# Optimization experiments

Hardware: AMD Instinct MI355X
Metric: run time of the kernel (lower is better)

## Reference

```python
import jax, jax.numpy as jnp
import numpy as np

U, P, D, H, E = 512, 1024, 128, 256, 98304
N = U + P


def setup_inputs() -> dict:
    key = jax.random.key(0)
    ks = jax.random.split(key, 16)
    def nrm(k, shape, scale=0.05):
        return jax.random.normal(k, shape, jnp.float32) * scale
    z = lambda *s: jnp.zeros(s, jnp.float32)
    return {
        "user_ids": jnp.arange(U),
        "paper_ids": jnp.arange(P),
        "edge_index": jax.random.randint(ks[0], (2, E), 0, N),
        "user_paper_interactions": jax.random.uniform(ks[1], (U, P), jnp.float32),
        "user_emb": nrm(ks[2], (U, D), 1.0),   # nn.Embedding tables
        "paper_emb": nrm(ks[3], (P, D), 1.0),
        "W0": nrm(ks[4], (D, H)), "b0": z(H),   # GCNConv weights (stored [in,out])
        "W1": nrm(ks[5], (H, H)), "b1": z(H),
        "W2": nrm(ks[6], (H, H)), "b2": z(H),
        "Wu": nrm(ks[7], (H, D)), "bu": z(D),   # user_output Linear
        "Wp": nrm(ks[8], (H, D)), "bp": z(D),   # paper_output Linear
        "Wq1": nrm(ks[9], (2 * D, H)), "bq1": z(H),  # predictor Linear 1
        "Wq2": nrm(ks[10], (H, 1)), "bq2": z(1),      # predictor Linear 2
    }


def gcn_conv(x, src, dst, W, b):
    """PyG GCNConv: add self-loops, symmetric D^-1/2 (A+I) D^-1/2 normalization."""
    n = x.shape[0]
    loop = jnp.arange(n)
    s = jnp.concatenate([src, loop])
    d = jnp.concatenate([dst, loop])
    deg = jax.ops.segment_sum(jnp.ones(d.shape, x.dtype), d, num_segments=n)
    dis = jnp.where(deg > 0, jax.lax.rsqrt(jnp.maximum(deg, 1.0)), 0.0)
    norm = dis[s] * dis[d]                      # [E+n]
    h = x @ W                                   # [n, H]
    out = jax.ops.segment_sum(h[s] * norm[:, None], d, num_segments=n)
    return out + b


def reference(user_ids, paper_ids, edge_index, user_paper_interactions,
              user_emb, paper_emb, W0, b0, W1, b1, W2, b2,
              Wu, bu, Wp, bp, Wq1, bq1, Wq2, bq2):
    # embedding lookups + node feature matrix [U+P, D]
    x = jnp.concatenate([user_emb[user_ids], paper_emb[paper_ids]], axis=0)
    src, dst = edge_index[0], edge_index[1]
    for W, b in ((W0, b0), (W1, b1), (W2, b2)):
        x = jax.nn.relu(gcn_conv(x, src, dst, W, b))  # dropout is identity in eval
    nu = user_ids.shape[0]
    np_ = paper_ids.shape[0]
    user_final = x[:nu] @ Wu + bu               # [U, D]
    paper_final = x[nu:] @ Wp + bp              # [P, D]
    # broadcast outer-product concat -> [U, P, 2D]
    combined = jnp.concatenate([
        jnp.broadcast_to(user_final[:, None, :], (nu, np_, user_final.shape[-1])),
        jnp.broadcast_to(paper_final[None, :, :], (nu, np_, paper_final.shape[-1])),
    ], axis=-1)
    h = jax.nn.relu(combined @ Wq1 + bq1)       # [U, P, H]
    pred = jax.nn.sigmoid(h @ Wq2 + bq2)[..., 0]  # [U, P]
    return pred
```

## Files before the change

### kernel.cpp

```cpp
#include <hip/hip_runtime.h>
#include <math.h>

constexpr int Uc = 512;
constexpr int Pc = 1024;
constexpr int Dc = 128;
constexpr int Hc = 256;
constexpr int Ec = 98304;
constexpr int Nc = 1536;
constexpr int CAP = 192;

__device__ __forceinline__ void fma4(float4& a, float n, const float4 r) {
    a.x += n * r.x; a.y += n * r.y; a.z += n * r.z; a.w += n * r.w;
}

template <int K>
__device__ __forceinline__ void gemm_core16(const float* __restrict__ xr,
                                            const float* __restrict__ wc, int M,
                                            float& acc0, float& acc1) {
#pragma unroll 4
    for (int k = 0; k < K; k += 4) {
        float4 a = *(const float4*)(xr + k);
        float2 b0 = *(const float2*)(wc + (size_t)k * M);
        float2 b1 = *(const float2*)(wc + (size_t)(k + 1) * M);
        float2 b2 = *(const float2*)(wc + (size_t)(k + 2) * M);
        float2 b3 = *(const float2*)(wc + (size_t)(k + 3) * M);
        acc0 += a.x * b0.x; acc1 += a.x * b0.y;
        acc0 += a.y * b1.x; acc1 += a.y * b1.y;
        acc0 += a.z * b2.x; acc1 += a.z * b2.y;
        acc0 += a.w * b3.x; acc1 += a.w * b3.y;
    }
}

__global__ void k_front(const int* __restrict__ e_src, const int* __restrict__ e_dst,
                        int* __restrict__ cnt, int* __restrict__ colF,
                        const float* __restrict__ Wu, const float* __restrict__ Wp,
                        const float* __restrict__ Wq1, const float* __restrict__ bu,
                        const float* __restrict__ bp, const float* __restrict__ bq1,
                        float* __restrict__ Wup, float* __restrict__ Wpp,
                        float* __restrict__ bvu, float* __restrict__ bvp) {
    int t = threadIdx.x, b = blockIdx.x;
    if (b < 384) {
        int e = b * 256 + t;
        int d = e_dst[e];
        int pos = atomicAdd(&cnt[d], 1);
        if (pos < CAP) colF[d * CAP + pos] = e_src[e];
    } else if (b < 640) {
        int id = b - 384;
        int z = id >> 7, tile = id & 127;
        int tx = t & 15, ty = t >> 4;
        const float* X = z ? Wp : Wu;
        const float* W = Wq1 + (z ? (size_t)Dc * Hc : 0);
        float* Y = z ? Wpp : Wup;
        int row = (tile >> 3) * 16 + ty, col = (tile & 7) * 32 + tx * 2;
        float a0 = 0.f, a1 = 0.f;
        gemm_core16<Dc>(X + (size_t)row * Dc, W + col, Hc, a0, a1);
        *(float2*)&Y[(size_t)row * Hc + col] = make_float2(a0, a1);
    } else if (b == 640) {
        float s = bq1[t];
#pragma unroll 8
        for (int d = 0; d < Dc; d++) s += bu[d] * Wq1[d * Hc + t];
        bvu[t] = s;
    } else {
        float s = 0.f;
#pragma unroll 8
        for (int d = 0; d < Dc; d++) s += bp[d] * Wq1[(Dc + d) * Hc + t];
        bvp[t] = s;
    }
}

__global__ void __launch_bounds__(256) k_l0(
        const int* __restrict__ uid, const int* __restrict__ pid,
        const float* __restrict__ ue, const float* __restrict__ pe,
        const float* __restrict__ W0, const float* __restrict__ b0,
        const int* __restrict__ cnt, const int* __restrict__ colF,
        float* __restrict__ out) {
    __shared__ const float* sptr[2][CAP];
    __shared__ float snrm[2][CAP];
    __shared__ __align__(16) float pagg[4][Dc];
    __shared__ __align__(16) float aggT[Dc][2];
    __shared__ __align__(16) float red[4][2][Hc];
    int t = threadIdx.x, b = blockIdx.x;
    int ibase = b * 2;
    int c[2]; float di[2];
#pragma unroll
    for (int r = 0; r < 2; r++) {
        c[r] = cnt[ibase + r];
        di[r] = rsqrtf((float)(c[r] + 1));
        int deg = min(c[r], CAP);
        if (t < deg) {
            int s = colF[(ibase + r) * CAP + t];
            sptr[r][t] = (s < Uc) ? ue + (size_t)uid[s] * Dc
                                  : pe + (size_t)pid[s - Uc] * Dc;
            snrm[r][t] = rsqrtf((float)(cnt[s] + 1));
        }
    }
    __syncthreads();
    {
        int wv = t >> 6, ln = t & 63;
        int r = wv >> 1, h = wv & 1;
        int i = ibase + r;
        int dg = min(c[r], CAP);
        int dg2 = dg >> 1;
        int j0 = h ? dg2 : 0, j1 = h ? dg : dg2;
        float2 acc = make_float2(0.f, 0.f);
        if (h == 0) {
            const float* xi = (i < Uc) ? ue + (size_t)uid[i] * Dc
                                       : pe + (size_t)pid[i - Uc] * Dc;
            float2 a2 = *(const float2*)(xi + ln * 2);
            acc.x = di[r] * a2.x;
            acc.y = di[r] * a2.y;
        }
        int j = j0;
        for (; j + 8 <= j1; j += 8) {
            float n0 = snrm[r][j],     n1 = snrm[r][j + 1];
            float n2 = snrm[r][j + 2], n3 = snrm[r][j + 3];
            float n4 = snrm[r][j + 4], n5 = snrm[r][j + 5];
            float n6 = snrm[r][j + 6], n7 = snrm[r][j + 7];
            float2 r0 = *(const float2*)(sptr[r][j]     + ln * 2);
            float2 r1 = *(const float2*)(sptr[r][j + 1] + ln * 2);
            float2 r2 = *(const float2*)(sptr[r][j + 2] + ln * 2);
            float2 r3 = *(const float2*)(sptr[r][j + 3] + ln * 2);
            float2 r4 = *(const float2*)(sptr[r][j + 4] + ln * 2);
            float2 r5 = *(const float2*)(sptr[r][j + 5] + ln * 2);
            float2 r6 = *(const float2*)(sptr[r][j + 6] + ln * 2);
            float2 r7 = *(const float2*)(sptr[r][j + 7] + ln * 2);
            acc.x += n0 * r0.x + n1 * r1.x + n2 * r2.x + n3 * r3.x;
            acc.y += n0 * r0.y + n1 * r1.y + n2 * r2.y + n3 * r3.y;
            acc.x += n4 * r4.x + n5 * r5.x + n6 * r6.x + n7 * r7.x;
            acc.y += n4 * r4.y + n5 * r5.y + n6 * r6.y + n7 * r7.y;
        }
        for (; j + 4 <= j1; j += 4) {
            float n0 = snrm[r][j],     n1 = snrm[r][j + 1];
            float n2 = snrm[r][j + 2], n3 = snrm[r][j + 3];
            float2 r0 = *(const float2*)(sptr[r][j]     + ln * 2);
            float2 r1 = *(const float2*)(sptr[r][j + 1] + ln * 2);
            float2 r2 = *(const float2*)(sptr[r][j + 2] + ln * 2);
            float2 r3 = *(const float2*)(sptr[r][j + 3] + ln * 2);
            acc.x += n0 * r0.x + n1 * r1.x + n2 * r2.x + n3 * r3.x;
            acc.y += n0 * r0.y + n1 * r1.y + n2 * r2.y + n3 * r3.y;
        }
        for (; j < j1; j++) {
            float2 r0 = *(const float2*)(sptr[r][j] + ln * 2);
            acc.x += snrm[r][j] * r0.x;
            acc.y += snrm[r][j] * r0.y;
        }
        pagg[wv][ln * 2]     = acc.x;
        pagg[wv][ln * 2 + 1] = acc.y;
    }
    __syncthreads();
    {
        int r = t >> 7, f = t & 127;
        aggT[f][r] = di[r] * (pagg[2 * r][f] + pagg[2 * r + 1][f]);
    }
    __syncthreads();
    {
        int wv = t >> 6, ln = t & 63;
        int k0 = wv * (Dc / 4);
        float4 a0 = {0.f, 0.f, 0.f, 0.f}, a1 = {0.f, 0.f, 0.f, 0.f};
        const float* Wp_ = W0 + (size_t)k0 * Hc + ln * 4;
#pragma unroll 8
        for (int kk = 0; kk < Dc / 4; kk++) {
            float2 g = *(const float2*)&aggT[k0 + kk][0];
            float4 w = *(const float4*)(Wp_ + (size_t)kk * Hc);
            a0.x += g.x * w.x; a0.y += g.x * w.y; a0.z += g.x * w.z; a0.w += g.x * w.w;
            a1.x += g.y * w.x; a1.y += g.y * w.y; a1.z += g.y * w.z; a1.w += g.y * w.w;
        }
        *(float4*)&red[wv][0][ln * 4] = a0;
        *(float4*)&red[wv][1][ln * 4] = a1;
    }
    __syncthreads();
    {
        float bb = b0[t];
        float s0 = (red[0][0][t] + red[1][0][t]) + (red[2][0][t] + red[3][0][t]) + bb;
        float s1 = (red[0][1][t] + red[1][1][t]) + (red[2][1][t] + red[3][1][t]) + bb;
        out[(size_t)(ibase + 0) * Hc + t] = fmaxf(s0, 0.f);
        out[(size_t)(ibase + 1) * Hc + t] = fmaxf(s1, 0.f);
    }
}

__device__ __forceinline__ void agg_wave2(const float* __restrict__ X,
                                          const int (*sidx)[CAP], const float (*snrm)[CAP],
                                          const int* c, const float* di, int ibase,
                                          float (*pagg)[Hc], int t) {
    int wv = t >> 6, ln = t & 63;
    int r = wv >> 1, h = wv & 1;
    int dg = min(c[r], CAP);
    int dg2 = dg >> 1;
    int j0 = h ? dg2 : 0, j1 = h ? dg : dg2;
    float4 acc = make_float4(0.f, 0.f, 0.f, 0.f);
    if (h == 0) {
        acc = *(const float4*)&X[(size_t)(ibase + r) * Hc + ln * 4];
        acc.x *= di[r]; acc.y *= di[r]; acc.z *= di[r]; acc.w *= di[r];
    }
    int j = j0;
    for (; j + 8 <= j1; j += 8) {
        float n0 = snrm[r][j],     n1 = snrm[r][j + 1];
        float n2 = snrm[r][j + 2], n3 = snrm[r][j + 3];
        float n4 = snrm[r][j + 4], n5 = snrm[r][j + 5];
        float n6 = snrm[r][j + 6], n7 = snrm[r][j + 7];
        float4 r0 = *(const float4*)&X[sidx[r][j]     + ln * 4];
        float4 r1 = *(const float4*)&X[sidx[r][j + 1] + ln * 4];
        float4 r2 = *(const float4*)&X[sidx[r][j + 2] + ln * 4];
        float4 r3 = *(const float4*)&X[sidx[r][j + 3] + ln * 4];
        float4 r4 = *(const float4*)&X[sidx[r][j + 4] + ln * 4];
        float4 r5 = *(const float4*)&X[sidx[r][j + 5] + ln * 4];
        float4 r6 = *(const float4*)&X[sidx[r][j + 6] + ln * 4];
        float4 r7 = *(const float4*)&X[sidx[r][j + 7] + ln * 4];
        fma4(acc, n0, r0); fma4(acc, n1, r1); fma4(acc, n2, r2); fma4(acc, n3, r3);
        fma4(acc, n4, r4); fma4(acc, n5, r5); fma4(acc, n6, r6); fma4(acc, n7, r7);
    }
    for (; j + 4 <= j1; j += 4) {
        float n0 = snrm[r][j],     n1 = snrm[r][j + 1];
        float n2 = snrm[r][j + 2], n3 = snrm[r][j + 3];
        float4 r0 = *(const float4*)&X[sidx[r][j]     + ln * 4];
        float4 r1 = *(const float4*)&X[sidx[r][j + 1] + ln * 4];
        float4 r2 = *(const float4*)&X[sidx[r][j + 2] + ln * 4];
        float4 r3 = *(const float4*)&X[sidx[r][j + 3] + ln * 4];
        fma4(acc, n0, r0); fma4(acc, n1, r1); fma4(acc, n2, r2); fma4(acc, n3, r3);
    }
    for (; j < j1; j++) {
        float4 r0 = *(const float4*)&X[sidx[r][j] + ln * 4];
        fma4(acc, snrm[r][j], r0);
    }
    *(float4*)&pagg[wv][ln * 4] = acc;
}

__device__ __forceinline__ void gemv_wsplit(const float (*aggT)[2],
                                            const float* __restrict__ W,
                                            float (*red)[2][Hc], int t) {
    int wv = t >> 6, ln = t & 63;
    int k0 = wv * (Hc / 4);
    float4 a0 = {0.f, 0.f, 0.f, 0.f}, a1 = {0.f, 0.f, 0.f, 0.f};
    const float* Wp_ = W + (size_t)k0 * Hc + ln * 4;
#pragma unroll 8
    for (int kk = 0; kk < Hc / 4; kk++) {
        float2 g = *(const float2*)&aggT[k0 + kk][0];
        float4 w = *(const float4*)(Wp_ + (size_t)kk * Hc);
        a0.x += g.x * w.x; a0.y += g.x * w.y; a0.z += g.x * w.z; a0.w += g.x * w.w;
        a1.x += g.y * w.x; a1.y += g.y * w.y; a1.z += g.y * w.z; a1.w += g.y * w.w;
    }
    *(float4*)&red[wv][0][ln * 4] = a0;
    *(float4*)&red[wv][1][ln * 4] = a1;
}

__global__ void __launch_bounds__(256) k_lh(
        const float* __restrict__ X, const float* __restrict__ W,
        const float* __restrict__ bias, const int* __restrict__ cnt,
        const int* __restrict__ colF, float* __restrict__ out) {
    __shared__ int sidx[2][CAP];
    __shared__ float snrm[2][CAP];
    __shared__ __align__(16) float pagg[4][Hc];
    __shared__ __align__(16) float aggT[Hc][2];
    __shared__ __align__(16) float red[4][2][Hc];
    int t = threadIdx.x, b = blockIdx.x;
    int ibase = b * 2;
    int c[2]; float di[2];
#pragma unroll
    for (int r = 0; r < 2; r++) {
        c[r] = cnt[ibase + r];
        di[r] = rsqrtf((float)(c[r] + 1));
        int deg = min(c[r], CAP);
        if (t < deg) {
            int s = colF[(ibase + r) * CAP + t];
            sidx[r][t] = s * Hc;
            snrm[r][t] = rsqrtf((float)(cnt[s] + 1));
        }
    }
    __syncthreads();
    agg_wave2(X, sidx, snrm, c, di, ibase, pagg, t);
    __syncthreads();
    *(float2*)&aggT[t][0] = make_float2(di[0] * (pagg[0][t] + pagg[1][t]),
                                        di[1] * (pagg[2][t] + pagg[3][t]));
    __syncthreads();
    gemv_wsplit(aggT, W, red, t);
    __syncthreads();
    {
        float bb = bias[t];
        float s0 = (red[0][0][t] + red[1][0][t]) + (red[2][0][t] + red[3][0][t]) + bb;
        float s1 = (red[0][1][t] + red[1][1][t]) + (red[2][1][t] + red[3][1][t]) + bb;
        out[(size_t)(ibase + 0) * Hc + t] = fmaxf(s0, 0.f);
        out[(size_t)(ibase + 1) * Hc + t] = fmaxf(s1, 0.f);
    }
}

__global__ void __launch_bounds__(256) k_lht(
        const float* __restrict__ X, const float* __restrict__ W2,
        const float* __restrict__ b2, const int* __restrict__ cnt,
        const int* __restrict__ colF,
        const float* __restrict__ Wup, const float* __restrict__ Wpp,
        const float* __restrict__ bvu, const float* __restrict__ bvp,
        float* __restrict__ AuT, float* __restrict__ ApT) {
    __shared__ int sidx[2][CAP];
    __shared__ float snrm[2][CAP];
    __shared__ __align__(16) float pagg[4][Hc];
    __shared__ __align__(16) float aggT[Hc][2];
    __shared__ __align__(16) float xlocT[Hc][2];
    __shared__ __align__(16) float red[4][2][Hc];
    int t = threadIdx.x, b = blockIdx.x;
    int ibase = b * 2;
    int c[2]; float di[2];
#pragma unroll
    for (int r = 0; r < 2; r++) {
        c[r] = cnt[ibase + r];
        di[r] = rsqrtf((float)(c[r] + 1));
        int deg = min(c[r], CAP);
        if (t < deg) {
            int s = colF[(ibase + r) * CAP + t];
            sidx[r][t] = s * Hc;
            snrm[r][t] = rsqrtf((float)(cnt[s] + 1));
        }
    }
    __syncthreads();
    agg_wave2(X, sidx, snrm, c, di, ibase, pagg, t);
    __syncthreads();
    *(float2*)&aggT[t][0] = make_float2(di[0] * (pagg[0][t] + pagg[1][t]),
                                        di[1] * (pagg[2][t] + pagg[3][t]));
    __syncthreads();
    gemv_wsplit(aggT, W2, red, t);
    __syncthreads();
    {
        float bb = b2[t];
        float s0 = (red[0][0][t] + red[1][0][t]) + (red[2][0][t] + red[3][0][t]) + bb;
        float s1 = (red[0][1][t] + red[1][1][t]) + (red[2][1][t] + red[3][1][t]) + bb;
        *(float2*)&xlocT[t][0] = make_float2(fmaxf(s0, 0.f), fmaxf(s1, 0.f));
    }
    __syncthreads();
    {
        const float* Wsel = (b < 256) ? Wup : Wpp;
        gemv_wsplit(xlocT, Wsel, red, t);
    }
    __syncthreads();
    {
        const float* bsel = (b < 256) ? bvu : bvp;
        float* YT  = (b < 256) ? AuT : ApT;
        int ldy    = (b < 256) ? Uc : Pc;
        int rloc   = (b < 256) ? ibase : ibase - Uc;
        float bb = bsel[t];
        float s0 = (red[0][0][t] + red[1][0][t]) + (red[2][0][t] + red[3][0][t]) + bb;
        float s1 = (red[0][1][t] + red[1][1][t]) + (red[2][1][t] + red[3][1][t]) + bb;
        *(float2*)&YT[(size_t)t * ldy + rloc] = make_float2(s0, s1);
    }
}

__global__ void __launch_bounds__(256) k_pred(
        const float* __restrict__ AuT, const float* __restrict__ ApT,
        const float* __restrict__ Wq2, const float* __restrict__ bq2,
        float* __restrict__ out) {
    __shared__ float auS[Hc * 8];
    int t = threadIdx.x;
    int ub = blockIdx.x * 8, pb = blockIdx.y * 256;
#pragma unroll
    for (int i = t; i < Hc * 8; i += 256) {
        int k = i >> 3, u = i & 7;
        auS[i] = AuT[(size_t)k * Uc + ub + u];
    }
    __syncthreads();
    int wv = t >> 6, ln = t & 63;
    const float* app = ApT + pb + ln * 4;
    const float* aup = auS + wv * 2;
    float acc[2][4] = {};
#pragma unroll 4
    for (int k = 0; k < Hc; k++) {
        float w = Wq2[k];
        float2 a = *(const float2*)(aup + k * 8);
        float4 p = *(const float4*)(app + (size_t)k * Pc);
        acc[0][0] += fmaxf(a.x + p.x, 0.f) * w;
        acc[0][1] += fmaxf(a.x + p.y, 0.f) * w;
        acc[0][2] += fmaxf(a.x + p.z, 0.f) * w;
        acc[0][3] += fmaxf(a.x + p.w, 0.f) * w;
        acc[1][0] += fmaxf(a.y + p.x, 0.f) * w;
        acc[1][1] += fmaxf(a.y + p.y, 0.f) * w;
        acc[1][2] += fmaxf(a.y + p.z, 0.f) * w;
        acc[1][3] += fmaxf(a.y + p.w, 0.f) * w;
    }
    float bq = bq2[0];
#pragma unroll
    for (int r = 0; r < 2; r++) {
        int u = ub + wv * 2 + r;
        float4 o;
        o.x = 1.f / (1.f + __expf(-(acc[r][0] + bq)));
        o.y = 1.f / (1.f + __expf(-(acc[r][1] + bq)));
        o.z = 1.f / (1.f + __expf(-(acc[r][2] + bq)));
        o.w = 1.f / (1.f + __expf(-(acc[r][3] + bq)));
        *(float4*)&out[(size_t)u * Pc + pb + ln * 4] = o;
    }
}


extern "C" void kernel_launch(void* const* d_in, const int* in_sizes, int n_in,
                              void* d_out, int out_size, void* d_ws, size_t ws_size,
                              hipStream_t stream) {
    const int*   uid = (const int*)d_in[0];
    const int*   pid = (const int*)d_in[1];
    const int*   ei  = (const int*)d_in[2];
    const float* ue  = (const float*)d_in[4];
    const float* pe  = (const float*)d_in[5];
    const float* W0  = (const float*)d_in[6];  const float* b0 = (const float*)d_in[7];
    const float* W1  = (const float*)d_in[8];  const float* b1 = (const float*)d_in[9];
    const float* W2  = (const float*)d_in[10]; const float* b2 = (const float*)d_in[11];
    const float* Wu  = (const float*)d_in[12]; const float* bu = (const float*)d_in[13];
    const float* Wp  = (const float*)d_in[14]; const float* bp = (const float*)d_in[15];
    const float* Wq1 = (const float*)d_in[16]; const float* bq1 = (const float*)d_in[17];
    const float* Wq2 = (const float*)d_in[18]; const float* bq2 = (const float*)d_in[19];

    const int* e_src = ei;
    const int* e_dst = ei + Ec;

    char* w = (char*)d_ws;
    auto alloc = [&](size_t bytes) { char* p = w; w += (bytes + 255) & ~size_t(255); return p; };
    int*   cnt  = (int*)alloc(Nc * 4);
    int*   colF = (int*)alloc((size_t)Nc * CAP * 4);
    float* xA   = (float*)alloc((size_t)Nc * Hc * 4);
    float* xB   = (float*)alloc((size_t)Nc * Hc * 4);
    float* Wup  = (float*)alloc((size_t)Hc * Hc * 4);
    float* Wpp  = (float*)alloc((size_t)Hc * Hc * 4);
    float* bvu  = (float*)alloc(Hc * 4);
    float* bvp  = (float*)alloc(Hc * 4);
    float* AuT  = (float*)alloc((size_t)Hc * Uc * 4);
    float* ApT  = (float*)alloc((size_t)Hc * Pc * 4);
    float* pred = (float*)d_out;

    hipMemsetAsync(cnt, 0, Nc * 4, stream);
    k_front<<<642, 256, 0, stream>>>(e_src, e_dst, cnt, colF, Wu, Wp, Wq1,
                                     bu, bp, bq1, Wup, Wpp, bvu, bvp);
    k_l0<<<Nc / 2, 256, 0, stream>>>(uid, pid, ue, pe, W0, b0, cnt, colF, xA);
    k_lh<<<Nc / 2, 256, 0, stream>>>(xA, W1, b1, cnt, colF, xB);
    k_lht<<<Nc / 2, 256, 0, stream>>>(xB, W2, b2, cnt, colF, Wup, Wpp, bvu, bvp, AuT, ApT);
    k_pred<<<dim3(Uc / 8, Pc / 256), 256, 0, stream>>>(AuT, ApT, Wq2, bq2, pred);
}
```

Before: 192.6 us.

## Fuse all GCN stages into one persistent cooperative kernel with grid syncs

```diff
diff --git a/kernel.cpp b/kernel.cpp
--- a/kernel.cpp
+++ b/kernel.cpp
@@ -1,5 +1,8 @@
 #include <hip/hip_runtime.h>
+#include <hip/hip_cooperative_groups.h>
 #include <math.h>
+
+namespace cg = cooperative_groups;
 
 constexpr int Uc = 512;
 constexpr int Pc = 1024;
@@ -12,6 +15,27 @@
 __device__ __forceinline__ void fma4(float4& a, float n, const float4 r) {
     a.x += n * r.x; a.y += n * r.y; a.z += n * r.z; a.w += n * r.w;
 }
+
+union __align__(16) SharedU {
+    struct {
+        const float* sptr[2][CAP];
+        float snrm[2][CAP];
+        float pagg[4][Dc];
+        float aggT[Dc][2];
+        float red[4][2][Hc];
+    } l0;
+    struct {
+        int sidx[2][CAP];
+        float snrm[2][CAP];
+        float pagg[4][Hc];
+        float aggT[Hc][2];
+        float xlocT[Hc][2];
+        float red[4][2][Hc];
+    } lh;
+    struct {
+        float auS[Hc * 8];
+    } pr;
+};
 
 template <int K>
 __device__ __forceinline__ void gemm_core16(const float* __restrict__ xr,
@@ -31,14 +55,15 @@
     }
 }
 
-__global__ void k_front(const int* __restrict__ e_src, const int* __restrict__ e_dst,
-                        int* __restrict__ cnt, int* __restrict__ colF,
-                        const float* __restrict__ Wu, const float* __restrict__ Wp,
-                        const float* __restrict__ Wq1, const float* __restrict__ bu,
-                        const float* __restrict__ bp, const float* __restrict__ bq1,
-                        float* __restrict__ Wup, float* __restrict__ Wpp,
-                        float* __restrict__ bvu, float* __restrict__ bvp) {
-    int t = threadIdx.x, b = blockIdx.x;
+__device__ __forceinline__ void phase_front(
+        int b, int t,
+        const int* __restrict__ e_src, const int* __restrict__ e_dst,
+        int* __restrict__ cnt, int* __restrict__ colF,
+        const float* __restrict__ Wu, const float* __restrict__ Wp,
+        const float* __restrict__ Wq1, const float* __restrict__ bu,
+        const float* __restrict__ bp, const float* __restrict__ bq1,
+        float* __restrict__ Wup, float* __restrict__ Wpp,
+        float* __restrict__ bvu, float* __restrict__ bvp) {
     if (b < 384) {
         int e = b * 256 + t;
         int d = e_dst[e];
@@ -60,7 +85,7 @@
 #pragma unroll 8
         for (int d = 0; d < Dc; d++) s += bu[d] * Wq1[d * Hc + t];
         bvu[t] = s;
-    } else {
+    } else if (b == 641) {
         float s = 0.f;
 #pragma unroll 8
         for (int d = 0; d < Dc; d++) s += bp[d] * Wq1[(Dc + d) * Hc + t];
@@ -68,18 +93,12 @@
     }
 }
 
-__global__ void __launch_bounds__(256) k_l0(
+__device__ void phase_l0(SharedU& su, int b, int t,
         const int* __restrict__ uid, const int* __restrict__ pid,
         const float* __restrict__ ue, const float* __restrict__ pe,
         const float* __restrict__ W0, const float* __restrict__ b0,
         const int* __restrict__ cnt, const int* __restrict__ colF,
         float* __restrict__ out) {
-    __shared__ const float* sptr[2][CAP];
-    __shared__ float snrm[2][CAP];
-    __shared__ __align__(16) float pagg[4][Dc];
-    __shared__ __align__(16) float aggT[Dc][2];
-    __shared__ __align__(16) float red[4][2][Hc];
-    int t = threadIdx.x, b = blockIdx.x;
     int ibase = b * 2;
     int c[2]; float di[2];
 #pragma unroll
@@ -89,9 +108,9 @@
         int deg = min(c[r], CAP);
         if (t < deg) {
             int s = colF[(ibase + r) * CAP + t];
-            sptr[r][t] = (s < Uc) ? ue + (size_t)uid[s] * Dc
-                                  : pe + (size_t)pid[s - Uc] * Dc;
-            snrm[r][t] = rsqrtf((float)(cnt[s] + 1));
+            su.l0.sptr[r][t] = (s < Uc) ? ue + (size_t)uid[s] * Dc
+                                        : pe + (size_t)pid[s - Uc] * Dc;
+            su.l0.snrm[r][t] = rsqrtf((float)(cnt[s] + 1));
         }
     }
     __syncthreads();
@@ -112,45 +131,45 @@
         }
         int j = j0;
         for (; j + 8 <= j1; j += 8) {
-            float n0 = snrm[r][j],     n1 = snrm[r][j + 1];
-            float n2 = snrm[r][j + 2], n3 = snrm[r][j + 3];
-            float n4 = snrm[r][j + 4], n5 = snrm[r][j + 5];
-            float n6 = snrm[r][j + 6], n7 = snrm[r][j + 7];
-            float2 r0 = *(const float2*)(sptr[r][j]     + ln * 2);
-            float2 r1 = *(const float2*)(sptr[r][j + 1] + ln * 2);
-            float2 r2 = *(const float2*)(sptr[r][j + 2] + ln * 2);
-            float2 r3 = *(const float2*)(sptr[r][j + 3] + ln * 2);
-            float2 r4 = *(const float2*)(sptr[r][j + 4] + ln * 2);
-            float2 r5 = *(const float2*)(sptr[r][j + 5] + ln * 2);
-            float2 r6 = *(const float2*)(sptr[r][j + 6] + ln * 2);
-            float2 r7 = *(const float2*)(sptr[r][j + 7] + ln * 2);
+            float n0 = su.l0.snrm[r][j],     n1 = su.l0.snrm[r][j + 1];
+            float n2 = su.l0.snrm[r][j + 2], n3 = su.l0.snrm[r][j + 3];
+            float n4 = su.l0.snrm[r][j + 4], n5 = su.l0.snrm[r][j + 5];
+            float n6 = su.l0.snrm[r][j + 6], n7 = su.l0.snrm[r][j + 7];
+            float2 r0 = *(const float2*)(su.l0.sptr[r][j]     + ln * 2);
+            float2 r1 = *(const float2*)(su.l0.sptr[r][j + 1] + ln * 2);
+            float2 r2 = *(const float2*)(su.l0.sptr[r][j + 2] + ln * 2);
+            float2 r3 = *(const float2*)(su.l0.sptr[r][j + 3] + ln * 2);
+            float2 r4 = *(const float2*)(su.l0.sptr[r][j + 4] + ln * 2);
+            float2 r5 = *(const float2*)(su.l0.sptr[r][j + 5] + ln * 2);
+            float2 r6 = *(const float2*)(su.l0.sptr[r][j + 6] + ln * 2);
+            float2 r7 = *(const float2*)(su.l0.sptr[r][j + 7] + ln * 2);
             acc.x += n0 * r0.x + n1 * r1.x + n2 * r2.x + n3 * r3.x;
             acc.y += n0 * r0.y + n1 * r1.y + n2 * r2.y + n3 * r3.y;
             acc.x += n4 * r4.x + n5 * r5.x + n6 * r6.x + n7 * r7.x;
             acc.y += n4 * r4.y + n5 * r5.y + n6 * r6.y + n7 * r7.y;
         }
         for (; j + 4 <= j1; j += 4) {
-            float n0 = snrm[r][j],     n1 = snrm[r][j + 1];
-            float n2 = snrm[r][j + 2], n3 = snrm[r][j + 3];
-            float2 r0 = *(const float2*)(sptr[r][j]     + ln * 2);
-            float2 r1 = *(const float2*)(sptr[r][j + 1] + ln * 2);
-            float2 r2 = *(const float2*)(sptr[r][j + 2] + ln * 2);
-            float2 r3 = *(const float2*)(sptr[r][j + 3] + ln * 2);
+            float n0 = su.l0.snrm[r][j],     n1 = su.l0.snrm[r][j + 1];
+            float n2 = su.l0.snrm[r][j + 2], n3 = su.l0.snrm[r][j + 3];
+            float2 r0 = *(const float2*)(su.l0.sptr[r][j]     + ln * 2);
+            float2 r1 = *(const float2*)(su.l0.sptr[r][j + 1] + ln * 2);
+            float2 r2 = *(const float2*)(su.l0.sptr[r][j + 2] + ln * 2);
+            float2 r3 = *(const float2*)(su.l0.sptr[r][j + 3] + ln * 2);
             acc.x += n0 * r0.x + n1 * r1.x + n2 * r2.x + n3 * r3.x;
             acc.y += n0 * r0.y + n1 * r1.y + n2 * r2.y + n3 * r3.y;
         }
         for (; j < j1; j++) {
-            float2 r0 = *(const float2*)(sptr[r][j] + ln * 2);
-            acc.x += snrm[r][j] * r0.x;
-            acc.y += snrm[r][j] * r0.y;
-        }
-        pagg[wv][ln * 2]     = acc.x;
-        pagg[wv][ln * 2 + 1] = acc.y;
+            float2 r0 = *(const float2*)(su.l0.sptr[r][j] + ln * 2);
+            acc.x += su.l0.snrm[r][j] * r0.x;
+            acc.y += su.l0.snrm[r][j] * r0.y;
+        }
+        su.l0.pagg[wv][ln * 2]     = acc.x;
+        su.l0.pagg[wv][ln * 2 + 1] = acc.y;
     }
     __syncthreads();
     {
         int r = t >> 7, f = t & 127;
-        aggT[f][r] = di[r] * (pagg[2 * r][f] + pagg[2 * r + 1][f]);
+        su.l0.aggT[f][r] = di[r] * (su.l0.pagg[2 * r][f] + su.l0.pagg[2 * r + 1][f]);
     }
     __syncthreads();
     {
@@ -160,19 +179,21 @@
         const float* Wp_ = W0 + (size_t)k0 * Hc + ln * 4;
 #pragma unroll 8
         for (int kk = 0; kk < Dc / 4; kk++) {
-            float2 g = *(const float2*)&aggT[k0 + kk][0];
+            float2 g = *(const float2*)&su.l0.aggT[k0 + kk][0];
             float4 w = *(const float4*)(Wp_ + (size_t)kk * Hc);
             a0.x += g.x * w.x; a0.y += g.x * w.y; a0.z += g.x * w.z; a0.w += g.x * w.w;
             a1.x += g.y * w.x; a1.y += g.y * w.y; a1.z += g.y * w.z; a1.w += g.y * w.w;
         }
-        *(float4*)&red[wv][0][ln * 4] = a0;
-        *(float4*)&red[wv][1][ln * 4] = a1;
+        *(float4*)&su.l0.red[wv][0][ln * 4] = a0;
+        *(float4*)&su.l0.red[wv][1][ln * 4] = a1;
     }
     __syncthreads();
     {
         float bb = b0[t];
-        float s0 = (red[0][0][t] + red[1][0][t]) + (red[2][0][t] + red[3][0][t]) + bb;
-        float s1 = (red[0][1][t] + red[1][1][t]) + (red[2][1][t] + red[3][1][t]) + bb;
+        float s0 = (su.l0.red[0][0][t] + su.l0.red[1][0][t]) +
+                   (su.l0.red[2][0][t] + su.l0.red[3][0][t]) + bb;
+        float s1 = (su.l0.red[0][1][t] + su.l0.red[1][1][t]) +
+                   (su.l0.red[2][1][t] + su.l0.red[3][1][t]) + bb;
         out[(size_t)(ibase + 0) * Hc + t] = fmaxf(s0, 0.f);
         out[(size_t)(ibase + 1) * Hc + t] = fmaxf(s1, 0.f);
     }
@@ -243,18 +264,10 @@
     *(float4*)&red[wv][1][ln * 4] = a1;
 }
 
-__global__ void __launch_bounds__(256) k_lh(
-        const float* __restrict__ X, const float* __restrict__ W,
-        const float* __restrict__ bias, const int* __restrict__ cnt,
-        const int* __restrict__ colF, float* __restrict__ out) {
-    __shared__ int sidx[2][CAP];
-    __shared__ float snrm[2][CAP];
-    __shared__ __align__(16) float pagg[4][Hc];
-    __shared__ __align__(16) float aggT[Hc][2];
-    __shared__ __align__(16) float red[4][2][Hc];
-    int t = threadIdx.x, b = blockIdx.x;
+__device__ __forceinline__ void layer_head(SharedU& su, int b, int t,
+        const float* __restrict__ X, const int* __restrict__ cnt,
+        const int* __restrict__ colF, int* c, float* di) {
     int ibase = b * 2;
-    int c[2]; float di[2];
 #pragma unroll
     for (int r = 0; r < 2; r++) {
         c[r] = cnt[ibase + r];
@@ -262,25 +275,168 @@
         int deg = min(c[r], CAP);
         if (t < deg) {
             int s = colF[(ibase + r) * CAP + t];
-            sidx[r][t] = s * Hc;
-            snrm[r][t] = rsqrtf((float)(cnt[s] + 1));
-        }
-    }
-    __syncthreads();
-    agg_wave2(X, sidx, snrm, c, di, ibase, pagg, t);
-    __syncthreads();
-    *(float2*)&aggT[t][0] = make_float2(di[0] * (pagg[0][t] + pagg[1][t]),
-                                        di[1] * (pagg[2][t] + pagg[3][t]));
-    __syncthreads();
-    gemv_wsplit(aggT, W, red, t);
-    __syncthreads();
-    {
-        float bb = bias[t];
-        float s0 = (red[0][0][t] + red[1][0][t]) + (red[2][0][t] + red[3][0][t]) + bb;
-        float s1 = (red[0][1][t] + red[1][1][t]) + (red[2][1][t] + red[3][1][t]) + bb;
-        out[(size_t)(ibase + 0) * Hc + t] = fmaxf(s0, 0.f);
-        out[(size_t)(ibase + 1) * Hc + t] = fmaxf(s1, 0.f);
-    }
+            su.lh.sidx[r][t] = s * Hc;
+            su.lh.snrm[r][t] = rsqrtf((float)(cnt[s] + 1));
+        }
+    }
+    __syncthreads();
+    agg_wave2(X, su.lh.sidx, su.lh.snrm, c, di, ibase, su.lh.pagg, t);
+    __syncthreads();
+    *(float2*)&su.lh.aggT[t][0] =
+        make_float2(di[0] * (su.lh.pagg[0][t] + su.lh.pagg[1][t]),
+                    di[1] * (su.lh.pagg[2][t] + su.lh.pagg[3][t]));
+    __syncthreads();
+}
+
+__device__ void phase_lh(SharedU& su, int b, int t,
+        const float* __restrict__ X, const float* __restrict__ W,
+        const float* __restrict__ bias, const int* __restrict__ cnt,
+        const int* __restrict__ colF, float* __restrict__ out) {
+    int c[2]; float di[2];
+    layer_head(su, b, t, X, cnt, colF, c, di);
+    gemv_wsplit(su.lh.aggT, W, su.lh.red, t);
+    __syncthreads();
+    int ibase = b * 2;
+    float bb = bias[t];
+    float s0 = (su.lh.red[0][0][t] + su.lh.red[1][0][t]) +
+               (su.lh.red[2][0][t] + su.lh.red[3][0][t]) + bb;
+    float s1 = (su.lh.red[0][1][t] + su.lh.red[1][1][t]) +
+               (su.lh.red[2][1][t] + su.lh.red[3][1][t]) + bb;
+    out[(size_t)(ibase + 0) * Hc + t] = fmaxf(s0, 0.f);
+    out[(size_t)(ibase + 1) * Hc + t] = fmaxf(s1, 0.f);
+}
+
+__device__ void phase_lht(SharedU& su, int b, int t,
+        const float* __restrict__ X, const float* __restrict__ W2,
+        const float* __restrict__ b2, const int* __restrict__ cnt,
+        const int* __restrict__ colF,
+        const float* __restrict__ Wup, const float* __restrict__ Wpp,
+        const float* __restrict__ bvu, const float* __restrict__ bvp,
+        float* __restrict__ AuT, float* __restrict__ ApT) {
+    int c[2]; float di[2];
+    layer_head(su, b, t, X, cnt, colF, c, di);
+    gemv_wsplit(su.lh.aggT, W2, su.lh.red, t);
+    __syncthreads();
+    {
+        float bb = b2[t];
+        float s0 = (su.lh.red[0][0][t] + su.lh.red[1][0][t]) +
+                   (su.lh.red[2][0][t] + su.lh.red[3][0][t]) + bb;
+        float s1 = (su.lh.red[0][1][t] + su.lh.red[1][1][t]) +
+                   (su.lh.red[2][1][t] + su.lh.red[3][1][t]) + bb;
+        *(float2*)&su.lh.xlocT[t][0] = make_float2(fmaxf(s0, 0.f), fmaxf(s1, 0.f));
+    }
+    __syncthreads();
+    gemv_wsplit(su.lh.xlocT, (b < 256) ? Wup : Wpp, su.lh.red, t);
+    __syncthreads();
+    {
+        int ibase = b * 2;
+        const float* bsel = (b < 256) ? bvu : bvp;
+        float* YT  = (b < 256) ? AuT : ApT;
+        int ldy    = (b < 256) ? Uc : Pc;
+        int rloc   = (b < 256) ? ibase : ibase - Uc;
+        float bb = bsel[t];
+        float s0 = (su.lh.red[0][0][t] + su.lh.red[1][0][t]) +
+                   (su.lh.red[2][0][t] + su.lh.red[3][0][t]) + bb;
+        float s1 = (su.lh.red[0][1][t] + su.lh.red[1][1][t]) +
+                   (su.lh.red[2][1][t] + su.lh.red[3][1][t]) + bb;
+        *(float2*)&YT[(size_t)t * ldy + rloc] = make_float2(s0, s1);
+    }
+}
+
+__device__ void phase_pred(float* auS, int b, int t,
+        const float* __restrict__ AuT, const float* __restrict__ ApT,
+        const float* __restrict__ Wq2, const float* __restrict__ bq2,
+        float* __restrict__ out) {
+    int ub = (b >> 3) * 8, pb = (b & 7) * 128;
+#pragma unroll
+    for (int i = t; i < Hc * 8; i += 256) {
+        int k = i >> 3, u = i & 7;
+        auS[i] = AuT[(size_t)k * Uc + ub + u];
+    }
+    __syncthreads();
+    int wv = t >> 6, ln = t & 63;
+    const float* app = ApT + pb + ln * 2;
+    const float* aup = auS + wv * 2;
+    float acc[2][2] = {};
+#pragma unroll 4
+    for (int k = 0; k < Hc; k++) {
+        float w = Wq2[k];
+        float2 a = *(const float2*)(aup + k * 8);
+        float2 p = *(const float2*)(app + (size_t)k * Pc);
+        acc[0][0] += fmaxf(a.x + p.x, 0.f) * w;
+        acc[0][1] += fmaxf(a.x + p.y, 0.f) * w;
+        acc[1][0] += fmaxf(a.y + p.x, 0.f) * w;
+        acc[1][1] += fmaxf(a.y + p.y, 0.f) * w;
+    }
+    float bq = bq2[0];
+#pragma unroll
+    for (int r = 0; r < 2; r++) {
+        int u = ub + wv * 2 + r;
+        float2 o;
+        o.x = 1.f / (1.f + __expf(-(acc[r][0] + bq)));
+        o.y = 1.f / (1.f + __expf(-(acc[r][1] + bq)));
+        *(float2*)&out[(size_t)u * Pc + pb + ln * 2] = o;
+    }
+}
+
+struct KArgs {
+    const int *uid, *pid, *e_src, *e_dst;
+    const float *ue, *pe;
+    const float *W0, *b0, *W1, *b1, *W2, *b2;
+    const float *Wu, *bu, *Wp, *bp, *Wq1, *bq1, *Wq2, *bq2;
+    int *cnt, *colF;
+    float *xA, *xB, *Wup, *Wpp, *bvu, *bvp, *AuT, *ApT, *pred;
+};
+
+__global__ void __launch_bounds__(256, 3) k_all(KArgs A) {
+    cg::grid_group g = cg::this_grid();
+    __shared__ SharedU su;
+    int t = threadIdx.x, b = blockIdx.x;
+    {
+        int i = b * 256 + t;
+        if (i < Nc) A.cnt[i] = 0;
+    }
+    g.sync();
+    phase_front(b, t, A.e_src, A.e_dst, A.cnt, A.colF, A.Wu, A.Wp, A.Wq1,
+                A.bu, A.bp, A.bq1, A.Wup, A.Wpp, A.bvu, A.bvp);
+    g.sync();
+    phase_l0(su, b, t, A.uid, A.pid, A.ue, A.pe, A.W0, A.b0, A.cnt, A.colF, A.xA);
+    g.sync();
+    phase_lh(su, b, t, A.xA, A.W1, A.b1, A.cnt, A.colF, A.xB);
+    g.sync();
+    phase_lht(su, b, t, A.xB, A.W2, A.b2, A.cnt, A.colF,
+              A.Wup, A.Wpp, A.bvu, A.bvp, A.AuT, A.ApT);
+    g.sync();
+    if (b < 512) phase_pred(su.pr.auS, b, t, A.AuT, A.ApT, A.Wq2, A.bq2, A.pred);
+}
+
+__global__ void k_front(const int* __restrict__ e_src, const int* __restrict__ e_dst,
+                        int* __restrict__ cnt, int* __restrict__ colF,
+                        const float* __restrict__ Wu, const float* __restrict__ Wp,
+                        const float* __restrict__ Wq1, const float* __restrict__ bu,
+                        const float* __restrict__ bp, const float* __restrict__ bq1,
+                        float* __restrict__ Wup, float* __restrict__ Wpp,
+                        float* __restrict__ bvu, float* __restrict__ bvp) {
+    phase_front(blockIdx.x, threadIdx.x, e_src, e_dst, cnt, colF, Wu, Wp, Wq1,
+                bu, bp, bq1, Wup, Wpp, bvu, bvp);
+}
+
+__global__ void __launch_bounds__(256) k_l0(
+        const int* __restrict__ uid, const int* __restrict__ pid,
+        const float* __restrict__ ue, const float* __restrict__ pe,
+        const float* __restrict__ W0, const float* __restrict__ b0,
+        const int* __restrict__ cnt, const int* __restrict__ colF,
+        float* __restrict__ out) {
+    __shared__ SharedU su;
+    phase_l0(su, blockIdx.x, threadIdx.x, uid, pid, ue, pe, W0, b0, cnt, colF, out);
+}
+
+__global__ void __launch_bounds__(256) k_lh(
+        const float* __restrict__ X, const float* __restrict__ W,
+        const float* __restrict__ bias, const int* __restrict__ cnt,
+        const int* __restrict__ colF, float* __restrict__ out) {
+    __shared__ SharedU su;
+    phase_lh(su, blockIdx.x, threadIdx.x, X, W, bias, cnt, colF, out);
 }
 
 __global__ void __launch_bounds__(256) k_lht(
@@ -290,141 +446,65 @@
         const float* __restrict__ Wup, const float* __restrict__ Wpp,
         const float* __restrict__ bvu, const float* __restrict__ bvp,
         float* __restrict__ AuT, float* __restrict__ ApT) {
-    __shared__ int sidx[2][CAP];
-    __shared__ float snrm[2][CAP];
-    __shared__ __align__(16) float pagg[4][Hc];
-    __shared__ __align__(16) float aggT[Hc][2];
-    __shared__ __align__(16) float xlocT[Hc][2];
-    __shared__ __align__(16) float red[4][2][Hc];
-    int t = threadIdx.x, b = blockIdx.x;
-    int ibase = b * 2;
-    int c[2]; float di[2];
-#pragma unroll
-    for (int r = 0; r < 2; r++) {
-        c[r] = cnt[ibase + r];
-        di[r] = rsqrtf((float)(c[r] + 1));
-        int deg = min(c[r], CAP);
-        if (t < deg) {
-            int s = colF[(ibase + r) * CAP + t];
-            sidx[r][t] = s * Hc;
-            snrm[r][t] = rsqrtf((float)(cnt[s] + 1));
-        }
-    }
-    __syncthreads();
-    agg_wave2(X, sidx, snrm, c, di, ibase, pagg, t);
-    __syncthreads();
-    *(float2*)&aggT[t][0] = make_float2(di[0] * (pagg[0][t] + pagg[1][t]),
-                                        di[1] * (pagg[2][t] + pagg[3][t]));
-    __syncthreads();
-    gemv_wsplit(aggT, W2, red, t);
-    __syncthreads();
-    {
-        float bb = b2[t];
-        float s0 = (red[0][0][t] + red[1][0][t]) + (red[2][0][t] + red[3][0][t]) + bb;
-        float s1 = (red[0][1][t] + red[1][1][t]) + (red[2][1][t] + red[3][1][t]) + bb;
-        *(float2*)&xlocT[t][0] = make_float2(fmaxf(s0, 0.f), fmaxf(s1, 0.f));
-    }
-    __syncthreads();
-    {
-        const float* Wsel = (b < 256) ? Wup : Wpp;
-        gemv_wsplit(xlocT, Wsel, red, t);
-    }
-    __syncthreads();
-    {
-        const float* bsel = (b < 256) ? bvu : bvp;
-        float* YT  = (b < 256) ? AuT : ApT;
-        int ldy    = (b < 256) ? Uc : Pc;
-        int rloc   = (b < 256) ? ibase : ibase - Uc;
-        float bb = bsel[t];
-        float s0 = (red[0][0][t] + red[1][0][t]) + (red[2][0][t] + red[3][0][t]) + bb;
-        float s1 = (red[0][1][t] + red[1][1][t]) + (red[2][1][t] + red[3][1][t]) + bb;
-        *(float2*)&YT[(size_t)t * ldy + rloc] = make_float2(s0, s1);
-    }
+    __shared__ SharedU su;
+    phase_lht(su, blockIdx.x, threadIdx.x, X, W2, b2, cnt, colF,
+              Wup, Wpp, bvu, bvp, AuT, ApT);
 }
 
 __global__ void __launch_bounds__(256) k_pred(
         const float* __restrict__ AuT, const float* __restrict__ ApT,
         const float* __restrict__ Wq2, const float* __restrict__ bq2,
         float* __restrict__ out) {
-    __shared__ float auS[Hc * 8];
-    int t = threadIdx.x;
-    int ub = blockIdx.x * 8, pb = blockIdx.y * 256;
-#pragma unroll
-    for (int i = t; i < Hc * 8; i += 256) {
-        int k = i >> 3, u = i & 7;
-        auS[i] = AuT[(size_t)k * Uc + ub + u];
-    }
-    __syncthreads();
-    int wv = t >> 6, ln = t & 63;
-    const float* app = ApT + pb + ln * 4;
-    const float* aup = auS + wv * 2;
-    float acc[2][4] = {};
-#pragma unroll 4
-    for (int k = 0; k < Hc; k++) {
-        float w = Wq2[k];
-        float2 a = *(const float2*)(aup + k * 8);
-        float4 p = *(const float4*)(app + (size_t)k * Pc);
-        acc[0][0] += fmaxf(a.x + p.x, 0.f) * w;
-        acc[0][1] += fmaxf(a.x + p.y, 0.f) * w;
-        acc[0][2] += fmaxf(a.x + p.z, 0.f) * w;
-        acc[0][3] += fmaxf(a.x + p.w, 0.f) * w;
-        acc[1][0] += fmaxf(a.y + p.x, 0.f) * w;
-        acc[1][1] += fmaxf(a.y + p.y, 0.f) * w;
-        acc[1][2] += fmaxf(a.y + p.z, 0.f) * w;
-        acc[1][3] += fmaxf(a.y + p.w, 0.f) * w;
-    }
-    float bq = bq2[0];
-#pragma unroll
-    for (int r = 0; r < 2; r++) {
-        int u = ub + wv * 2 + r;
-        float4 o;
-        o.x = 1.f / (1.f + __expf(-(acc[r][0] + bq)));
-        o.y = 1.f / (1.f + __expf(-(acc[r][1] + bq)));
-        o.z = 1.f / (1.f + __expf(-(acc[r][2] + bq)));
-        o.w = 1.f / (1.f + __expf(-(acc[r][3] + bq)));
-        *(float4*)&out[(size_t)u * Pc + pb + ln * 4] = o;
-    }
-}
-
+    __shared__ SharedU su;
+    phase_pred(su.pr.auS, blockIdx.x, threadIdx.x, AuT, ApT, Wq2, bq2, out);
+}
 
 extern "C" void kernel_launch(void* const* d_in, const int* in_sizes, int n_in,
                               void* d_out, int out_size, void* d_ws, size_t ws_size,
                               hipStream_t stream) {
-    const int*   uid = (const int*)d_in[0];
-    const int*   pid = (const int*)d_in[1];
-    const int*   ei  = (const int*)d_in[2];
-    const float* ue  = (const float*)d_in[4];
-    const float* pe  = (const float*)d_in[5];
-    const float* W0  = (const float*)d_in[6];  const float* b0 = (const float*)d_in[7];
-    const float* W1  = (const float*)d_in[8];  const float* b1 = (const float*)d_in[9];
-    const float* W2  = (const float*)d_in[10]; const float* b2 = (const float*)d_in[11];
-    const float* Wu  = (const float*)d_in[12]; const float* bu = (const float*)d_in[13];
-    const float* Wp  = (const float*)d_in[14]; const float* bp = (const float*)d_in[15];
-    const float* Wq1 = (const float*)d_in[16]; const float* bq1 = (const float*)d_in[17];
-    const float* Wq2 = (const float*)d_in[18]; const float* bq2 = (const float*)d_in[19];
-
-    const int* e_src = ei;
-    const int* e_dst = ei + Ec;
+    KArgs A;
+    A.uid = (const int*)d_in[0];
+    A.pid = (const int*)d_in[1];
+    const int* ei = (const int*)d_in[2];
+    A.e_src = ei;
+    A.e_dst = ei + Ec;
+    A.ue  = (const float*)d_in[4];
+    A.pe  = (const float*)d_in[5];
+    A.W0  = (const float*)d_in[6];  A.b0  = (const float*)d_in[7];
+    A.W1  = (const float*)d_in[8];  A.b1  = (const float*)d_in[9];
+    A.W2  = (const float*)d_in[10]; A.b2  = (const float*)d_in[11];
+    A.Wu  = (const float*)d_in[12]; A.bu  = (const float*)d_in[13];
+    A.Wp  = (const float*)d_in[14]; A.bp  = (const float*)d_in[15];
+    A.Wq1 = (const float*)d_in[16]; A.bq1 = (const float*)d_in[17];
+    A.Wq2 = (const float*)d_in[18]; A.bq2 = (const float*)d_in[19];
 
     char* w = (char*)d_ws;
     auto alloc = [&](size_t bytes) { char* p = w; w += (bytes + 255) & ~size_t(255); return p; };
-    int*   cnt  = (int*)alloc(Nc * 4);
-    int*   colF = (int*)alloc((size_t)Nc * CAP * 4);
-    float* xA   = (float*)alloc((size_t)Nc * Hc * 4);
-    float* xB   = (float*)alloc((size_t)Nc * Hc * 4);
-    float* Wup  = (float*)alloc((size_t)Hc * Hc * 4);
-    float* Wpp  = (float*)alloc((size_t)Hc * Hc * 4);
-    float* bvu  = (float*)alloc(Hc * 4);
-    float* bvp  = (float*)alloc(Hc * 4);
-    float* AuT  = (float*)alloc((size_t)Hc * Uc * 4);
-    float* ApT  = (float*)alloc((size_t)Hc * Pc * 4);
-    float* pred = (float*)d_out;
-
-    hipMemsetAsync(cnt, 0, Nc * 4, stream);
-    k_front<<<642, 256, 0, stream>>>(e_src, e_dst, cnt, colF, Wu, Wp, Wq1,
-                                     bu, bp, bq1, Wup, Wpp, bvu, bvp);
-    k_l0<<<Nc / 2, 256, 0, stream>>>(uid, pid, ue, pe, W0, b0, cnt, colF, xA);
-    k_lh<<<Nc / 2, 256, 0, stream>>>(xA, W1, b1, cnt, colF, xB);
-    k_lht<<<Nc / 2, 256, 0, stream>>>(xB, W2, b2, cnt, colF, Wup, Wpp, bvu, bvp, AuT, ApT);
-    k_pred<<<dim3(Uc / 8, Pc / 256), 256, 0, stream>>>(AuT, ApT, Wq2, bq2, pred);
-}
+    A.cnt  = (int*)alloc(Nc * 4);
+    A.colF = (int*)alloc((size_t)Nc * CAP * 4);
+    A.xA   = (float*)alloc((size_t)Nc * Hc * 4);
+    A.xB   = (float*)alloc((size_t)Nc * Hc * 4);
+    A.Wup  = (float*)alloc((size_t)Hc * Hc * 4);
+    A.Wpp  = (float*)alloc((size_t)Hc * Hc * 4);
+    A.bvu  = (float*)alloc(Hc * 4);
+    A.bvp  = (float*)alloc(Hc * 4);
+    A.AuT  = (float*)alloc((size_t)Hc * Uc * 4);
+    A.ApT  = (float*)alloc((size_t)Hc * Pc * 4);
+    A.pred = (float*)d_out;
+
+    void* kargs[] = { (void*)&A };
+    hipError_t err = hipLaunchCooperativeKernel((void*)k_all, dim3(768), dim3(256),
+                                                kargs, 0, stream);
+    if (err == hipSuccess) return;
+
+    hipMemsetAsync(A.cnt, 0, Nc * 4, stream);
+    k_front<<<642, 256, 0, stream>>>(A.e_src, A.e_dst, A.cnt, A.colF, A.Wu, A.Wp,
+                                     A.Wq1, A.bu, A.bp, A.bq1, A.Wup, A.Wpp,
+                                     A.bvu, A.bvp);
+    k_l0<<<Nc / 2, 256, 0, stream>>>(A.uid, A.pid, A.ue, A.pe, A.W0, A.b0,
+                                     A.cnt, A.colF, A.xA);
+    k_lh<<<Nc / 2, 256, 0, stream>>>(A.xA, A.W1, A.b1, A.cnt, A.colF, A.xB);
+    k_lht<<<Nc / 2, 256, 0, stream>>>(A.xB, A.W2, A.b2, A.cnt, A.colF,
+                                      A.Wup, A.Wpp, A.bvu, A.bvp, A.AuT, A.ApT);
+    k_pred<<<512, 256, 0, stream>>>(A.AuT, A.ApT, A.Wq2, A.bq2, A.pred);
+}
```

Result: slower. 690.8 us (+258.6%).
